# Kernel optimization log

Hardware: AMD Instinct MI355X
Metric: run time of the kernel (lower is better)

The kernel has to match this reference:

```python
import jax, jax.numpy as jnp
import numpy as np

ENC_DIM = 128
DEC_DIM = 128
NUM_HEADS = 4
HEAD_DIM = DEC_DIM // NUM_HEADS


def _layernorm(x, g, b, eps=1e-5):
    mu = jnp.mean(x, axis=-1, keepdims=True)
    var = jnp.mean((x - mu) ** 2, axis=-1, keepdims=True)
    return (x - mu) * jax.lax.rsqrt(var + eps) * g + b


def setup_inputs() -> dict:
    key = jax.random.key(0)
    ks = jax.random.split(key, 12)
    B, H, W, D = 2, 16, 16, 16
    s = 0.02
    return {
        "encoder_feat": jax.random.normal(ks[0], (B, ENC_DIM, H, W, D), jnp.float32),
        "decoder_feat": jax.random.normal(ks[1], (B, DEC_DIM, H, W, D), jnp.float32),
        # torch Linear weights stored as [out, in]
        "Wq": jax.random.normal(ks[2], (DEC_DIM, DEC_DIM), jnp.float32) * s,
        "bq": jnp.zeros((DEC_DIM,), jnp.float32),
        "Wk": jax.random.normal(ks[3], (DEC_DIM, ENC_DIM), jnp.float32) * s,
        "bk": jnp.zeros((DEC_DIM,), jnp.float32),
        "Wv": jax.random.normal(ks[4], (DEC_DIM, ENC_DIM), jnp.float32) * s,
        "bv": jnp.zeros((DEC_DIM,), jnp.float32),
        "Wo": jax.random.normal(ks[5], (DEC_DIM, DEC_DIM), jnp.float32) * s,
        "bo": jnp.zeros((DEC_DIM,), jnp.float32),
        "g_enc": jnp.ones((ENC_DIM,), jnp.float32),
        "b_enc": jnp.zeros((ENC_DIM,), jnp.float32),
        "g_dec": jnp.ones((DEC_DIM,), jnp.float32),
        "b_dec": jnp.zeros((DEC_DIM,), jnp.float32),
        "g_out": jnp.ones((DEC_DIM,), jnp.float32),
        "b_out": jnp.zeros((DEC_DIM,), jnp.float32),
        "W1": jax.random.normal(ks[6], (DEC_DIM * 4, DEC_DIM), jnp.float32) * s,
        "b1": jnp.zeros((DEC_DIM * 4,), jnp.float32),
        "W2": jax.random.normal(ks[7], (DEC_DIM, DEC_DIM * 4), jnp.float32) * s,
        "b2": jnp.zeros((DEC_DIM,), jnp.float32),
    }


def reference(encoder_feat, decoder_feat, Wq, bq, Wk, bk, Wv, bv, Wo, bo,
              g_enc, b_enc, g_dec, b_dec, g_out, b_out, W1, b1, W2, b2):
    B, C_dec, H, W_, D = decoder_feat.shape
    N = H * W_ * D
    scale = HEAD_DIM ** -0.5
    # [B, C, H, W, D] -> [B, N, C]
    enc_seq = encoder_feat.reshape(B, -1, N).transpose(0, 2, 1)
    dec_seq = decoder_feat.reshape(B, C_dec, N).transpose(0, 2, 1)
    enc_seq = _layernorm(enc_seq, g_enc, b_enc)
    dec_seq = _layernorm(dec_seq, g_dec, b_dec)
    # projections (torch Linear: x @ W.T + b), split heads -> [B, h, N, d]
    Q = (dec_seq @ Wq.T + bq).reshape(B, N, NUM_HEADS, HEAD_DIM).transpose(0, 2, 1, 3)
    K = (enc_seq @ Wk.T + bk).reshape(B, N, NUM_HEADS, HEAD_DIM).transpose(0, 2, 1, 3)
    V = (enc_seq @ Wv.T + bv).reshape(B, N, NUM_HEADS, HEAD_DIM).transpose(0, 2, 1, 3)
    attn = jnp.einsum('bhqd,bhkd->bhqk', Q, K) * scale  # [B, h, N, N]
    attn = jax.nn.softmax(attn, axis=-1)
    out = jnp.einsum('bhqk,bhkd->bhqd', attn, V)
    out = out.transpose(0, 2, 1, 3).reshape(B, N, C_dec)
    out = out @ Wo.T + bo
    out = dec_seq + out
    h = _layernorm(out, g_out, b_out)
    ffn = jax.nn.gelu(h @ W1.T + b1, approximate=False) @ W2.T + b2
    out = out + ffn
    return out.transpose(0, 2, 1).reshape(B, C_dec, H, W_, D)
```

## Files before the change

### kernel.cpp

```cpp
#include <hip/hip_runtime.h>
#include <hip/hip_bf16.h>
#include <math.h>

#define B_ 2
#define N_ 4096
#define BN_ 8192
#define NH_ 4
#define SPLIT_ 8

using bf16x8   = __attribute__((ext_vector_type(8))) __bf16;
using f32x4    = __attribute__((ext_vector_type(4))) float;
using ushortx8 = __attribute__((ext_vector_type(8))) unsigned short;

#if __has_builtin(__builtin_amdgcn_exp2f)
#define FAST_EXP2(x) __builtin_amdgcn_exp2f(x)
#else
#define FAST_EXP2(x) __expf((x) * 0.6931471805599453f)
#endif

static __device__ __forceinline__ unsigned short f2bf(float f) {
    union { __hip_bfloat16 h; unsigned short u; } c;
    c.h = __float2bfloat16(f);
    return c.u;
}
static __device__ __forceinline__ float bf2f(unsigned short u) {
    union { __hip_bfloat16 h; unsigned short u; } c;
    c.u = u;
    return __bfloat162float(c.h);
}
static __device__ __forceinline__ unsigned int pk2bf(float lo, float hi) {
    return __builtin_amdgcn_perm(__float_as_uint(hi) + 0x8000u,
                                 __float_as_uint(lo) + 0x8000u, 0x07060302u);
}

__global__ __launch_bounds__(256)
void convert_weights_kernel(const float* __restrict__ Wq, const float* __restrict__ Wk,
                            const float* __restrict__ Wv, const float* __restrict__ Wo,
                            const float* __restrict__ W1, const float* __restrict__ W2,
                            unsigned short* __restrict__ wq, unsigned short* __restrict__ wk,
                            unsigned short* __restrict__ wv, unsigned short* __restrict__ wo,
                            unsigned short* __restrict__ w1, unsigned short* __restrict__ w2) {
    const int id = blockIdx.x * 256 + threadIdx.x;
    if      (id <  16384) wq[id]          = f2bf(Wq[id]);
    else if (id <  32768) wk[id - 16384]  = f2bf(Wk[id - 16384]);
    else if (id <  49152) wv[id - 32768]  = f2bf(Wv[id - 32768]);
    else if (id <  65536) wo[id - 49152]  = f2bf(Wo[id - 49152]);
    else if (id < 131072) w1[id - 65536]  = f2bf(W1[id - 65536]);
    else                  w2[id - 131072] = f2bf(W2[id - 131072]);
}

__global__ __launch_bounds__(128)
void qkv_ln_kernel(const float* __restrict__ enc, const float* __restrict__ dec,
                   const float* __restrict__ g_enc, const float* __restrict__ b_enc,
                   const float* __restrict__ g_dec, const float* __restrict__ b_dec,
                   const unsigned short* __restrict__ wq,
                   const unsigned short* __restrict__ wk,
                   const unsigned short* __restrict__ wv,
                   const float* __restrict__ bq, const float* __restrict__ bk,
                   const float* __restrict__ bv,
                   unsigned short* __restrict__ Qh, unsigned short* __restrict__ Kh,
                   unsigned short* __restrict__ Vt,
                   unsigned short* __restrict__ dec_lnb) {
    const int z    = blockIdx.y;
    const int half = blockIdx.z;
    const int t = threadIdx.x;
    const int wvx = t >> 6, lane = t & 63;
    const int l15 = lane & 15, quad = lane >> 4;
    const int m0 = blockIdx.x * 32 + wvx * 16;
    const int b = m0 >> 12, n0 = m0 & 4095;
    const float* inb   = ((z == 0) ? dec : enc) + (size_t)b * 128 * N_;
    const float* gamma = (z == 0) ? g_dec : g_enc;
    const float* beta  = (z == 0) ? b_dec : b_enc;
    const unsigned short* Wb = (z == 0) ? wq : (z == 1) ? wk : wv;
    const float* bias        = (z == 0) ? bq : (z == 1) ? bk : bv;

    float x[4][8];
    float s = 0.f, ss = 0.f;
    #pragma unroll
    for (int kk = 0; kk < 4; ++kk) {
        #pragma unroll
        for (int j = 0; j < 8; ++j) {
            const int c = kk * 32 + quad * 8 + j;
            const float v = inb[(size_t)c * N_ + n0 + l15];
            x[kk][j] = v; s += v; ss += v * v;
        }
    }
    s  += __shfl_xor(s, 16);  s  += __shfl_xor(s, 32);
    ss += __shfl_xor(ss, 16); ss += __shfl_xor(ss, 32);
    const float mu  = s * (1.f / 128.f);
    const float inv = rsqrtf(ss * (1.f / 128.f) - mu * mu + 1e-5f);

    bf16x8 af[4];
    #pragma unroll
    for (int kk = 0; kk < 4; ++kk) {
        float y[8];
        #pragma unroll
        for (int j = 0; j < 8; ++j) {
            const int c = kk * 32 + quad * 8 + j;
            y[j] = (x[kk][j] - mu) * inv * gamma[c] + beta[c];
        }
        union { uint4 u; bf16x8 v8; ushortx8 us; } cvt;
        cvt.u.x = pk2bf(y[0], y[1]); cvt.u.y = pk2bf(y[2], y[3]);
        cvt.u.z = pk2bf(y[4], y[5]); cvt.u.w = pk2bf(y[6], y[7]);
        af[kk] = cvt.v8;
        if (z == 0 && half == 0)
            *(ushortx8*)(dec_lnb + (size_t)(m0 + l15) * 128 + kk * 32 + quad * 8) = cvt.us;
    }

    const float qsc = 0.17677669529663687f * 1.4426950408889634f;
    const int nb0 = n0 + quad * 4;
    #pragma unroll
    for (int nb = 0; nb < 4; ++nb) {
        const int col = half * 64 + nb * 16 + l15;
        f32x4 a = {0.f, 0.f, 0.f, 0.f};
        #pragma unroll
        for (int kk = 0; kk < 4; ++kk) {
            const bf16x8 wf = *(const bf16x8*)(Wb + (size_t)col * 128 + kk * 32 + quad * 8);
            a = __builtin_amdgcn_mfma_f32_16x16x32_bf16(af[kk], wf, a, 0, 0, 0);
        }
        const int h = col >> 5, d = col & 31;
        const float bz = bias[col];
        if (z == 2) {
            ushort4 pk;
            pk.x = f2bf(a[0] + bz);
            pk.y = f2bf(a[1] + bz);
            pk.z = f2bf(a[2] + bz);
            pk.w = f2bf(a[3] + bz);
            *(ushort4*)(Vt + ((size_t)(b * NH_ + h) * 32 + d) * N_ + nb0) = pk;
        } else {
            unsigned short* dst = (z == 0) ? Qh : Kh;
            const float sc = (z == 0) ? qsc : 1.f;
            #pragma unroll
            for (int r = 0; r < 4; ++r)
                dst[((size_t)(b * NH_ + h) * N_ + nb0 + r) * 32 + d] = f2bf((a[r] + bz) * sc);
        }
    }
}

__global__ __launch_bounds__(256)
void attn_kernel5(const unsigned short* __restrict__ Qh,
                  const unsigned short* __restrict__ Kh,
                  const unsigned short* __restrict__ Vt,
                  unsigned short* __restrict__ Op,
                  unsigned short* __restrict__ lp) {
    __shared__ alignas(16) unsigned short sP[4][64][72];

    const int gid   = blockIdx.x;
    const int combo = gid & 63;
    const int qblk  = gid >> 6;
    const int bh    = combo & 7;
    const int s     = combo >> 3;
    const int t  = threadIdx.x;
    const int wvx = t >> 6, lane = t & 63;
    const int l15 = lane & 15, quad = lane >> 4;
    const int qw = qblk * 256 + wvx * 64;
    const size_t hbse = (size_t)bh * N_ * 32;

    bf16x8 qf[4];
    #pragma unroll
    for (int f = 0; f < 4; ++f)
        qf[f] = *(const bf16x8*)(Qh + hbse + (size_t)(qw + f * 16 + l15) * 32 + quad * 8);

    const unsigned short* Kp = Kh + hbse;
    const unsigned short* Vp = Vt + (size_t)bh * 32 * N_;

    f32x4 o0[4], o1[4];
    float l[4];
    #pragma unroll
    for (int f = 0; f < 4; ++f) {
        o0[f] = f32x4{0.f, 0.f, 0.f, 0.f};
        o1[f] = f32x4{0.f, 0.f, 0.f, 0.f};
        l[f] = 0.f;
    }
    const f32x4 zero = {0.f, 0.f, 0.f, 0.f};

    const int kbeg = s * (N_ / SPLIT_);
    const int kend = kbeg + (N_ / SPLIT_);

    bf16x8 kf[4];
    #pragma unroll
    for (int c = 0; c < 4; ++c)
        kf[c] = *(const bf16x8*)(Kp + (size_t)(kbeg + c * 16 + l15) * 32 + quad * 8);

    for (int k0 = kbeg; k0 < kend; k0 += 64) {
        bf16x8 va[2], vb[2];
        #pragma unroll
        for (int s2 = 0; s2 < 2; ++s2) {
            va[s2] = *(const bf16x8*)(Vp + (size_t)l15 * N_        + k0 + s2 * 32 + quad * 8);
            vb[s2] = *(const bf16x8*)(Vp + (size_t)(16 + l15) * N_ + k0 + s2 * 32 + quad * 8);
        }
        const int kn = (k0 + 64 < kend) ? (k0 + 64) : kbeg;
        bf16x8 kfn[4];
        #pragma unroll
        for (int c = 0; c < 4; ++c)
            kfn[c] = *(const bf16x8*)(Kp + (size_t)(kn + c * 16 + l15) * 32 + quad * 8);

        #pragma unroll
        for (int f = 0; f < 4; ++f) {
            #pragma unroll
            for (int c = 0; c < 4; ++c) {
                const f32x4 sv = __builtin_amdgcn_mfma_f32_16x16x32_bf16(kf[c], qf[f], zero, 0, 0, 0);
                const float p0 = FAST_EXP2(sv[0]);
                const float p1 = FAST_EXP2(sv[1]);
                const float p2 = FAST_EXP2(sv[2]);
                const float p3 = FAST_EXP2(sv[3]);
                l[f] += (p0 + p1) + (p2 + p3);
                uint2 pk;
                pk.x = pk2bf(p0, p1);
                pk.y = pk2bf(p2, p3);
                *(uint2*)&sP[wvx][f * 16 + l15][c * 16 + quad * 4] = pk;
            }
        }
        #pragma unroll
        for (int f = 0; f < 4; ++f) {
            #pragma unroll
            for (int s2 = 0; s2 < 2; ++s2) {
                const bf16x8 pf = *(const bf16x8*)&sP[wvx][f * 16 + l15][s2 * 32 + quad * 8];
                o0[f] = __builtin_amdgcn_mfma_f32_16x16x32_bf16(va[s2], pf, o0[f], 0, 0, 0);
                o1[f] = __builtin_amdgcn_mfma_f32_16x16x32_bf16(vb[s2], pf, o1[f], 0, 0, 0);
            }
        }
        #pragma unroll
        for (int c = 0; c < 4; ++c) kf[c] = kfn[c];
    }

    #pragma unroll
    for (int f = 0; f < 4; ++f) {
        float lf = l[f];
        lf += __shfl_xor(lf, 16);
        lf += __shfl_xor(lf, 32);
        const int tok = qw + f * 16 + l15;
        const size_t ob = ((size_t)(s * 8 + bh) * N_ + tok) * 32;
        uint2 w0, w1v;
        w0.x  = pk2bf(o0[f][0], o0[f][1]); w0.y  = pk2bf(o0[f][2], o0[f][3]);
        w1v.x = pk2bf(o1[f][0], o1[f][1]); w1v.y = pk2bf(o1[f][2], o1[f][3]);
        *(uint2*)&Op[ob + quad * 4]      = w0;
        *(uint2*)&Op[ob + 16 + quad * 4] = w1v;
        if (quad == 0)
            lp[(size_t)(s * 8 + bh) * N_ + tok] = f2bf(lf);
    }
}

__global__ __launch_bounds__(256)
void fused_tail2_kernel(const unsigned short* __restrict__ Op,
                        const unsigned short* __restrict__ lp,
                        const unsigned short* __restrict__ wo,
                        const float* __restrict__ bo,
                        const unsigned short* __restrict__ decb,
                        const float* __restrict__ g, const float* __restrict__ be,
                        const unsigned short* __restrict__ w1,
                        const float* __restrict__ b1,
                        const unsigned short* __restrict__ w2,
                        const float* __restrict__ b2,
                        float* __restrict__ out) {
    __shared__ alignas(16) float sred[4][64][32];
    __shared__ float sln[4][2][16];
    __shared__ alignas(16) unsigned short hb_lds[16][136];
    __shared__ alignas(16) unsigned short smid[16][536];
    const int t = threadIdx.x;
    const int wv = t >> 6, lane = t & 63;
    const int l15 = lane & 15, quad = lane >> 4;
    const int m0 = blockIdx.x * 16;

    const int tokA = m0 + l15;
    const int bA = tokA >> 12, nA = tokA & 4095;
    const int bhh = bA * NH_ + wv;
    bf16x8 af;
    {
        f32x4 sa = {0.f, 0.f, 0.f, 0.f}, sb = {0.f, 0.f, 0.f, 0.f};
        float lt = 0.f;
        #pragma unroll
        for (int s = 0; s < SPLIT_; ++s) {
            const size_t base = ((size_t)(s * 8 + bhh) * N_ + nA) * 32 + quad * 8;
            const ushortx8 u = *(const ushortx8*)&Op[base];
            sa[0] += bf2f(u[0]); sa[1] += bf2f(u[1]);
            sa[2] += bf2f(u[2]); sa[3] += bf2f(u[3]);
            sb[0] += bf2f(u[4]); sb[1] += bf2f(u[5]);
            sb[2] += bf2f(u[6]); sb[3] += bf2f(u[7]);
            lt += bf2f(lp[(size_t)(s * 8 + bhh) * N_ + nA]);
        }
        const float inv = 1.f / lt;
        union { uint4 u; bf16x8 v; } cvt;
        cvt.u.x = pk2bf(sa[0] * inv, sa[1] * inv);
        cvt.u.y = pk2bf(sa[2] * inv, sa[3] * inv);
        cvt.u.z = pk2bf(sb[0] * inv, sb[1] * inv);
        cvt.u.w = pk2bf(sb[2] * inv, sb[3] * inv);
        af = cvt.v;
    }

    #pragma unroll
    for (int nb = 0; nb < 8; ++nb) {
        const bf16x8 wf = *(const bf16x8*)(wo + (size_t)(nb * 16 + l15) * 128
                                           + wv * 32 + quad * 8);
        const f32x4 a = __builtin_amdgcn_mfma_f32_16x16x32_bf16(
            af, wf, f32x4{0.f, 0.f, 0.f, 0.f}, 0, 0, 0);
        *(f32x4*)&sred[wv][lane][nb * 4] = a;
    }
    __syncthreads();

    float v[2][4];
    #pragma unroll
    for (int lnb = 0; lnb < 2; ++lnb) {
        const int nbg = 2 * wv + lnb;
        f32x4 p = *(const f32x4*)&sred[0][lane][nbg * 4];
        p += *(const f32x4*)&sred[1][lane][nbg * 4];
        p += *(const f32x4*)&sred[2][lane][nbg * 4];
        p += *(const f32x4*)&sred[3][lane][nbg * 4];
        const int col = nbg * 16 + l15;
        const float bz = bo[col];
        #pragma unroll
        for (int r = 0; r < 4; ++r) {
            const int tok = m0 + quad * 4 + r;
            v[lnb][r] = p[r] + bz + bf2f(decb[(size_t)tok * 128 + col]);
        }
    }

    {
        float s[4], ss[4];
        #pragma unroll
        for (int r = 0; r < 4; ++r) {
            float a = v[0][r] + v[1][r];
            float b = v[0][r] * v[0][r] + v[1][r] * v[1][r];
            for (int m = 1; m < 16; m <<= 1) {
                a += __shfl_xor(a, m);
                b += __shfl_xor(b, m);
            }
            s[r] = a; ss[r] = b;
        }
        if (l15 == 0) {
            #pragma unroll
            for (int r = 0; r < 4; ++r) {
                sln[wv][0][quad * 4 + r] = s[r];
                sln[wv][1][quad * 4 + r] = ss[r];
            }
        }
    }
    __syncthreads();

    {
        #pragma unroll
        for (int r = 0; r < 4; ++r) {
            const int tk = quad * 4 + r;
            const float stot  = sln[0][0][tk] + sln[1][0][tk] + sln[2][0][tk] + sln[3][0][tk];
            const float sstot = sln[0][1][tk] + sln[1][1][tk] + sln[2][1][tk] + sln[3][1][tk];
            const float mu  = stot * (1.f / 128.f);
            const float inv = rsqrtf(sstot * (1.f / 128.f) - mu * mu + 1e-5f);
            #pragma unroll
            for (int lnb = 0; lnb < 2; ++lnb) {
                const int col = (2 * wv + lnb) * 16 + l15;
                hb_lds[tk][col] = f2bf((v[lnb][r] - mu) * inv * g[col] + be[col]);
            }
        }
    }
    __syncthreads();

    bf16x8 hf[4];
    #pragma unroll
    for (int kk = 0; kk < 4; ++kk)
        hf[kk] = *(const bf16x8*)&hb_lds[l15][kk * 32 + quad * 8];
    #pragma unroll
    for (int nb = 0; nb < 8; ++nb) {
        const int col = wv * 128 + nb * 16 + l15;
        f32x4 a = {0.f, 0.f, 0.f, 0.f};
        #pragma unroll
        for (int kk = 0; kk < 4; ++kk) {
            const bf16x8 wf = *(const bf16x8*)(w1 + (size_t)col * 128 + kk * 32 + quad * 8);
            a = __builtin_amdgcn_mfma_f32_16x16x32_bf16(hf[kk], wf, a, 0, 0, 0);
        }
        const float bz = b1[col];
        #pragma unroll
        for (int r = 0; r < 4; ++r) {
            float x = a[r] + bz;
            x = 0.5f * x * (1.f + erff(x * 0.70710678118f));
            smid[quad * 4 + r][col] = f2bf(x);
        }
    }
    __syncthreads();

    f32x4 acc[8];
    #pragma unroll
    for (int nb = 0; nb < 8; ++nb) acc[nb] = f32x4{0.f, 0.f, 0.f, 0.f};
    #pragma unroll
    for (int kk = 0; kk < 4; ++kk) {
        const bf16x8 af2 = *(const bf16x8*)&smid[l15][wv * 128 + kk * 32 + quad * 8];
        #pragma unroll
        for (int nb = 0; nb < 8; ++nb) {
            const bf16x8 wf = *(const bf16x8*)(w2 + (size_t)(nb * 16 + l15) * 512
                                               + wv * 128 + kk * 32 + quad * 8);
            acc[nb] = __builtin_amdgcn_mfma_f32_16x16x32_bf16(af2, wf, acc[nb], 0, 0, 0);
        }
    }
    #pragma unroll
    for (int nb = 0; nb < 8; ++nb)
        *(f32x4*)&sred[wv][lane][nb * 4] = acc[nb];
    __syncthreads();

    {
        const int b = m0 >> 12;
        const int nb0 = (m0 & 4095) + quad * 4;
        #pragma unroll
        for (int lnb = 0; lnb < 2; ++lnb) {
            const int nbg = 2 * wv + lnb;
            f32x4 p = *(const f32x4*)&sred[0][lane][nbg * 4];
            p += *(const f32x4*)&sred[1][lane][nbg * 4];
            p += *(const f32x4*)&sred[2][lane][nbg * 4];
            p += *(const f32x4*)&sred[3][lane][nbg * 4];
            const int col = nbg * 16 + l15;
            const float bz = b2[col];
            f32x4 res;
            #pragma unroll
            for (int r = 0; r < 4; ++r)
                res[r] = p[r] + bz + v[lnb][r];
            *(f32x4*)&out[((size_t)(b * 128 + col)) * N_ + nb0] = res;
        }
    }
}

extern "C" void kernel_launch(void* const* d_in, const int* in_sizes, int n_in,
                              void* d_out, int out_size, void* d_ws, size_t ws_size,
                              hipStream_t stream) {
    const float* enc   = (const float*)d_in[0];
    const float* dec   = (const float*)d_in[1];
    const float* Wq    = (const float*)d_in[2];
    const float* bq    = (const float*)d_in[3];
    const float* Wk    = (const float*)d_in[4];
    const float* bk    = (const float*)d_in[5];
    const float* Wv    = (const float*)d_in[6];
    const float* bv    = (const float*)d_in[7];
    const float* Wo    = (const float*)d_in[8];
    const float* bo    = (const float*)d_in[9];
    const float* g_enc = (const float*)d_in[10];
    const float* b_enc = (const float*)d_in[11];
    const float* g_dec = (const float*)d_in[12];
    const float* b_dec = (const float*)d_in[13];
    const float* g_out = (const float*)d_in[14];
    const float* b_out = (const float*)d_in[15];
    const float* W1    = (const float*)d_in[16];
    const float* b1    = (const float*)d_in[17];
    const float* W2    = (const float*)d_in[18];
    const float* b2    = (const float*)d_in[19];
    float* out = (float*)d_out;
    char*  W   = (char*)d_ws;

    unsigned short* wqb = (unsigned short*)(W);
    unsigned short* wkb = wqb + 16384;
    unsigned short* wvb = wkb + 16384;
    unsigned short* wob = wvb + 16384;
    unsigned short* w1b = wob + 16384;
    unsigned short* w2b = w1b + 65536;
    unsigned short* dec_lnb = (unsigned short*)(W + (2560ull << 10));
    unsigned short* Qh      = (unsigned short*)(W + (4608ull << 10));
    unsigned short* Kh      = (unsigned short*)(W + (6656ull << 10));
    unsigned short* Vt      = (unsigned short*)(W + (8704ull << 10));
    unsigned short* Op      = (unsigned short*)(W + (10752ull << 10));
    unsigned short* lpb     = (unsigned short*)(W + (27136ull << 10));

    convert_weights_kernel<<<768, 256, 0, stream>>>(Wq, Wk, Wv, Wo, W1, W2,
                                                    wqb, wkb, wvb, wob, w1b, w2b);

    qkv_ln_kernel<<<dim3(BN_ / 32, 3, 2), 128, 0, stream>>>(
        enc, dec, g_enc, b_enc, g_dec, b_dec, wqb, wkb, wvb,
        bq, bk, bv, Qh, Kh, Vt, dec_lnb);

    attn_kernel5<<<1024, 256, 0, stream>>>(Qh, Kh, Vt, Op, lpb);

    fused_tail2_kernel<<<512, 256, 0, stream>>>(Op, lpb, wob, bo, dec_lnb,
                                                g_out, b_out, w1b, b1, w2b, b2, out);
}
```

Baseline: 172.5 us.

## Share LayerNorm input tile across Q/K/V projections and shrink tail reduction buffer

The QKV kernel now loads each 32-token input tile into shared memory once and computes LayerNorm stats there. Each block covers all output columns, with z=0 producing Q and z=1 producing both K and V from one encoder load, instead of re-reading the input for every projection and column half. Separately, the tail kernel's cross-wave partial sums are stored in LDS as bf16 rather than fp32, shrinking shared memory at the cost of extra rounding and an added barrier. The bf16 partials add precision loss to the output-projection and FFN reductions.

New measurement: 167.6 us. 1.03x faster.

```diff
diff --git a/kernel.cpp b/kernel.cpp
--- a/kernel.cpp
+++ b/kernel.cpp
@@ -49,69 +49,95 @@
     else                  w2[id - 131072] = f2bf(W2[id - 131072]);
 }
 
-__global__ __launch_bounds__(128)
-void qkv_ln_kernel(const float* __restrict__ enc, const float* __restrict__ dec,
-                   const float* __restrict__ g_enc, const float* __restrict__ b_enc,
-                   const float* __restrict__ g_dec, const float* __restrict__ b_dec,
-                   const unsigned short* __restrict__ wq,
-                   const unsigned short* __restrict__ wk,
-                   const unsigned short* __restrict__ wv,
-                   const float* __restrict__ bq, const float* __restrict__ bk,
-                   const float* __restrict__ bv,
-                   unsigned short* __restrict__ Qh, unsigned short* __restrict__ Kh,
-                   unsigned short* __restrict__ Vt,
-                   unsigned short* __restrict__ dec_lnb) {
-    const int z    = blockIdx.y;
-    const int half = blockIdx.z;
-    const int t = threadIdx.x;
-    const int wvx = t >> 6, lane = t & 63;
-    const int l15 = lane & 15, quad = lane >> 4;
-    const int m0 = blockIdx.x * 32 + wvx * 16;
-    const int b = m0 >> 12, n0 = m0 & 4095;
+__global__ __launch_bounds__(256)
+void qkv2_kernel(const float* __restrict__ enc, const float* __restrict__ dec,
+                 const float* __restrict__ g_enc, const float* __restrict__ b_enc,
+                 const float* __restrict__ g_dec, const float* __restrict__ b_dec,
+                 const unsigned short* __restrict__ wq,
+                 const unsigned short* __restrict__ wk,
+                 const unsigned short* __restrict__ wv,
+                 const float* __restrict__ bq, const float* __restrict__ bk,
+                 const float* __restrict__ bv,
+                 unsigned short* __restrict__ Qh, unsigned short* __restrict__ Kh,
+                 unsigned short* __restrict__ Vt,
+                 unsigned short* __restrict__ dec_lnb) {
+    __shared__ float tile[128][33];
+    __shared__ float mu_s[32], inv_s[32];
+    const int z  = blockIdx.y;
+    const int t  = threadIdx.x;
+    const int m0 = blockIdx.x * 32;
+    const int b  = m0 >> 12, n0 = m0 & 4095;
     const float* inb   = ((z == 0) ? dec : enc) + (size_t)b * 128 * N_;
     const float* gamma = (z == 0) ? g_dec : g_enc;
     const float* beta  = (z == 0) ? b_dec : b_enc;
-    const unsigned short* Wb = (z == 0) ? wq : (z == 1) ? wk : wv;
-    const float* bias        = (z == 0) ? bq : (z == 1) ? bk : bv;
-
-    float x[4][8];
-    float s = 0.f, ss = 0.f;
+
+    {
+        const int col = t & 31;
+        const int r0  = t >> 5;
+        #pragma unroll
+        for (int j = 0; j < 16; ++j) {
+            const int r = r0 + 8 * j;
+            tile[r][col] = inb[(size_t)r * N_ + n0 + col];
+        }
+    }
+    __syncthreads();
+    {
+        const int tok = t >> 3;
+        const int ln  = t & 7;
+        float s = 0.f, ss = 0.f;
+        for (int c = ln; c < 128; c += 8) {
+            const float x = tile[c][tok];
+            s += x; ss += x * x;
+        }
+        for (int m = 1; m < 8; m <<= 1) {
+            s  += __shfl_xor(s, m);
+            ss += __shfl_xor(ss, m);
+        }
+        if (ln == 0) {
+            const float mu  = s * (1.f / 128.f);
+            mu_s[tok]  = mu;
+            inv_s[tok] = rsqrtf(ss * (1.f / 128.f) - mu * mu + 1e-5f);
+        }
+    }
+    __syncthreads();
+
+    const int wvx = t >> 6, lane = t & 63;
+    const int l15 = lane & 15, quad = lane >> 4;
+    const int tokgrp  = (wvx & 1) * 16;
+    const int colbase = (z == 0) ? (wvx >> 1) * 64 : 0;
+    const bool isV    = (z == 1) && (wvx >> 1);
+    const bool wrLN   = (z == 0) && ((wvx >> 1) == 0);
+    const int nbCount = (z == 0) ? 4 : 8;
+    const int tok = tokgrp + l15;
+    const float mu  = mu_s[tok];
+    const float inv = inv_s[tok];
+
+    bf16x8 af[4];
     #pragma unroll
     for (int kk = 0; kk < 4; ++kk) {
+        float y[8];
         #pragma unroll
         for (int j = 0; j < 8; ++j) {
             const int c = kk * 32 + quad * 8 + j;
-            const float v = inb[(size_t)c * N_ + n0 + l15];
-            x[kk][j] = v; s += v; ss += v * v;
-        }
-    }
-    s  += __shfl_xor(s, 16);  s  += __shfl_xor(s, 32);
-    ss += __shfl_xor(ss, 16); ss += __shfl_xor(ss, 32);
-    const float mu  = s * (1.f / 128.f);
-    const float inv = rsqrtf(ss * (1.f / 128.f) - mu * mu + 1e-5f);
-
-    bf16x8 af[4];
-    #pragma unroll
-    for (int kk = 0; kk < 4; ++kk) {
-        float y[8];
-        #pragma unroll
-        for (int j = 0; j < 8; ++j) {
-            const int c = kk * 32 + quad * 8 + j;
-            y[j] = (x[kk][j] - mu) * inv * gamma[c] + beta[c];
+            y[j] = (tile[c][tok] - mu) * inv * gamma[c] + beta[c];
         }
         union { uint4 u; bf16x8 v8; ushortx8 us; } cvt;
         cvt.u.x = pk2bf(y[0], y[1]); cvt.u.y = pk2bf(y[2], y[3]);
         cvt.u.z = pk2bf(y[4], y[5]); cvt.u.w = pk2bf(y[6], y[7]);
         af[kk] = cvt.v8;
-        if (z == 0 && half == 0)
-            *(ushortx8*)(dec_lnb + (size_t)(m0 + l15) * 128 + kk * 32 + quad * 8) = cvt.us;
-    }
-
-    const float qsc = 0.17677669529663687f * 1.4426950408889634f;
-    const int nb0 = n0 + quad * 4;
-    #pragma unroll
-    for (int nb = 0; nb < 4; ++nb) {
-        const int col = half * 64 + nb * 16 + l15;
+        if (wrLN)
+            *(ushortx8*)(dec_lnb + (size_t)(m0 + tok) * 128 + kk * 32 + quad * 8) = cvt.us;
+    }
+
+    const unsigned short* Wb = (z == 0) ? wq : (isV ? wv : wk);
+    const float* bias        = (z == 0) ? bq : (isV ? bv : bk);
+    const float sc = (z == 0) ? (0.17677669529663687f * 1.4426950408889634f) : 1.f;
+    const int nbase = n0 + tokgrp + quad * 4;
+
+    #pragma unroll
+    for (int nb = 0; nb < 8; ++nb) {
+        if (nb >= nbCount) break;
+        const int col = colbase + nb * 16 + l15;
         f32x4 a = {0.f, 0.f, 0.f, 0.f};
         #pragma unroll
         for (int kk = 0; kk < 4; ++kk) {
@@ -120,19 +146,18 @@
         }
         const int h = col >> 5, d = col & 31;
         const float bz = bias[col];
-        if (z == 2) {
+        if (isV) {
             ushort4 pk;
             pk.x = f2bf(a[0] + bz);
             pk.y = f2bf(a[1] + bz);
             pk.z = f2bf(a[2] + bz);
             pk.w = f2bf(a[3] + bz);
-            *(ushort4*)(Vt + ((size_t)(b * NH_ + h) * 32 + d) * N_ + nb0) = pk;
+            *(ushort4*)(Vt + ((size_t)(b * NH_ + h) * 32 + d) * N_ + nbase) = pk;
         } else {
             unsigned short* dst = (z == 0) ? Qh : Kh;
-            const float sc = (z == 0) ? qsc : 1.f;
             #pragma unroll
             for (int r = 0; r < 4; ++r)
-                dst[((size_t)(b * NH_ + h) * N_ + nb0 + r) * 32 + d] = f2bf((a[r] + bz) * sc);
+                dst[((size_t)(b * NH_ + h) * N_ + nbase + r) * 32 + d] = f2bf((a[r] + bz) * sc);
         }
     }
 }
@@ -242,7 +267,7 @@
 }
 
 __global__ __launch_bounds__(256)
-void fused_tail2_kernel(const unsigned short* __restrict__ Op,
+void fused_tail3_kernel(const unsigned short* __restrict__ Op,
                         const unsigned short* __restrict__ lp,
                         const unsigned short* __restrict__ wo,
                         const float* __restrict__ bo,
@@ -253,7 +278,7 @@
                         const unsigned short* __restrict__ w2,
                         const float* __restrict__ b2,
                         float* __restrict__ out) {
-    __shared__ alignas(16) float sred[4][64][32];
+    __shared__ alignas(16) unsigned short sredb[4][64][36];
     __shared__ float sln[4][2][16];
     __shared__ alignas(16) unsigned short hb_lds[16][136];
     __shared__ alignas(16) unsigned short smid[16][536];
@@ -294,7 +319,10 @@
                                            + wv * 32 + quad * 8);
         const f32x4 a = __builtin_amdgcn_mfma_f32_16x16x32_bf16(
             af, wf, f32x4{0.f, 0.f, 0.f, 0.f}, 0, 0, 0);
-        *(f32x4*)&sred[wv][lane][nb * 4] = a;
+        uint2 p;
+        p.x = pk2bf(a[0], a[1]);
+        p.y = pk2bf(a[2], a[3]);
+        *(uint2*)&sredb[wv][lane][nb * 4] = p;
     }
     __syncthreads();
 
@@ -302,10 +330,13 @@
     #pragma unroll
     for (int lnb = 0; lnb < 2; ++lnb) {
         const int nbg = 2 * wv + lnb;
-        f32x4 p = *(const f32x4*)&sred[0][lane][nbg * 4];
-        p += *(const f32x4*)&sred[1][lane][nbg * 4];
-        p += *(const f32x4*)&sred[2][lane][nbg * 4];
-        p += *(const f32x4*)&sred[3][lane][nbg * 4];
+        f32x4 p = {0.f, 0.f, 0.f, 0.f};
+        #pragma unroll
+        for (int w = 0; w < 4; ++w) {
+            const ushort4 u = *(const ushort4*)&sredb[w][lane][nbg * 4];
+            p[0] += bf2f(u.x); p[1] += bf2f(u.y);
+            p[2] += bf2f(u.z); p[3] += bf2f(u.w);
+        }
         const int col = nbg * 16 + l15;
         const float bz = bo[col];
         #pragma unroll
@@ -390,9 +421,14 @@
             acc[nb] = __builtin_amdgcn_mfma_f32_16x16x32_bf16(af2, wf, acc[nb], 0, 0, 0);
         }
     }
-    #pragma unroll
-    for (int nb = 0; nb < 8; ++nb)
-        *(f32x4*)&sred[wv][lane][nb * 4] = acc[nb];
+    __syncthreads();
+    #pragma unroll
+    for (int nb = 0; nb < 8; ++nb) {
+        uint2 p;
+        p.x = pk2bf(acc[nb][0], acc[nb][1]);
+        p.y = pk2bf(acc[nb][2], acc[nb][3]);
+        *(uint2*)&sredb[wv][lane][nb * 4] = p;
+    }
     __syncthreads();
 
     {
@@ -401,10 +437,13 @@
         #pragma unroll
         for (int lnb = 0; lnb < 2; ++lnb) {
             const int nbg = 2 * wv + lnb;
-            f32x4 p = *(const f32x4*)&sred[0][lane][nbg * 4];
-            p += *(const f32x4*)&sred[1][lane][nbg * 4];
-            p += *(const f32x4*)&sred[2][lane][nbg * 4];
-            p += *(const f32x4*)&sred[3][lane][nbg * 4];
+            f32x4 p = {0.f, 0.f, 0.f, 0.f};
+            #pragma unroll
+            for (int w = 0; w < 4; ++w) {
+                const ushort4 u = *(const ushort4*)&sredb[w][lane][nbg * 4];
+                p[0] += bf2f(u.x); p[1] += bf2f(u.y);
+                p[2] += bf2f(u.z); p[3] += bf2f(u.w);
+            }
             const int col = nbg * 16 + l15;
             const float bz = b2[col];
             f32x4 res;
@@ -458,12 +497,12 @@
     convert_weights_kernel<<<768, 256, 0, stream>>>(Wq, Wk, Wv, Wo, W1, W2,
                                                     wqb, wkb, wvb, wob, w1b, w2b);
 
-    qkv_ln_kernel<<<dim3(BN_ / 32, 3, 2), 128, 0, stream>>>(
+    qkv2_kernel<<<dim3(BN_ / 32, 2), 256, 0, stream>>>(
         enc, dec, g_enc, b_enc, g_dec, b_dec, wqb, wkb, wvb,
         bq, bk, bv, Qh, Kh, Vt, dec_lnb);
 
     attn_kernel5<<<1024, 256, 0, stream>>>(Qh, Kh, Vt, Op, lpb);
 
-    fused_tail2_kernel<<<512, 256, 0, stream>>>(Op, lpb, wob, bo, dec_lnb,
+    fused_tail3_kernel<<<512, 256, 0, stream>>>(Op, lpb, wob, bo, dec_lnb,
                                                 g_out, b_out, w1b, b1, w2b, b2, out);
 }
```
